# Optimization experiments

Hardware: AMD Instinct MI355X
Metric: run time of the kernel (lower is better)

Reference implementation:

```python
import jax, jax.numpy as jnp
import numpy as np

IN_DIM = 784
HIDDEN = 512
STYLE = 128
BATCH = 2048
NUM_LABELS = 10


def setup_inputs() -> dict:
    key = jax.random.key(0)
    k1, k2, k3, k4 = jax.random.split(key, 4)
    x = jax.random.uniform(k1, (BATCH, IN_DIM), dtype=jnp.float32)
    m = jax.random.randint(k2, (BATCH,), 0, NUM_LABELS)
    # Embedding tables, scaled as in the torch __init__ (N(0,1)/fan)
    fc1_table = jax.random.normal(k3, (NUM_LABELS, (IN_DIM + 1) * HIDDEN), dtype=jnp.float32) / ((IN_DIM + 1) * HIDDEN)
    fc2_table = jax.random.normal(k4, (NUM_LABELS, (HIDDEN + 1) * STYLE), dtype=jnp.float32) / ((HIDDEN + 1) * STYLE)
    return {"x": x, "m": m, "fc1_table": fc1_table, "fc2_table": fc2_table}


def reference(x, m, fc1_table, fc2_table):
    B = x.shape[0]
    x = x.reshape(B, -1)  # [B, 784]
    # Per-sample weight matrices gathered by label
    fc1 = fc1_table[m].reshape(B, IN_DIM + 1, HIDDEN)   # [B, 785, H]
    fc1_w, fc1_b = fc1[:, :IN_DIM, :], fc1[:, -1, :]
    h1 = jax.nn.relu(jnp.einsum('bkj,bk->bj', fc1_w, x) + fc1_b)  # [B, H]
    fc2 = fc2_table[m].reshape(B, HIDDEN + 1, STYLE)    # [B, H+1, S]
    fc2_w, fc2_b = fc2[:, :HIDDEN, :], fc2[:, -1, :]
    h2 = jnp.einsum('bkj,bk->bj', fc2_w, h1) + fc2_b    # [B, S]
    return jax.nn.sigmoid(h2)
```

## Files before the change

kernel.cpp:

```cpp
#include <hip/hip_runtime.h>
#include <hip/hip_bf16.h>
#include <math.h>

#define BATCH      2048
#define IN_DIM     784
#define HIDDEN     512
#define STYLE      128
#define NUM_LABELS 10
#define FC1_STRIDE ((IN_DIM + 1) * HIDDEN)
#define FC2_STRIDE ((HIDDEN + 1) * STYLE)
#define KP1        832
#define TB         64
#define BK         64
#define MAX_TILES  48

#define META_NTILES 31
#define META_TILES  32
#define META_PERM   176

#define W1B_OFF  16384ULL
#define W2B_OFF  (W1B_OFF + 10ULL*HIDDEN*KP1*2)
#define H1B_OFF  (W2B_OFF + 10ULL*STYLE*HIDDEN*2)
#define BF16_NEED (H1B_OFF + (size_t)BATCH*HIDDEN*2)

#define W1_KB 26
#define W1_NB 16
#define W2_KB 16
#define W2_NB 4
#define W1_BLOCKS (W1_KB*W1_NB*NUM_LABELS)
#define W2_BLOCKS (W2_KB*W2_NB*NUM_LABELS)

typedef short short8  __attribute__((ext_vector_type(8)));
typedef float float4e __attribute__((ext_vector_type(4)));

__device__ __forceinline__ ushort f2b(float v) {
    __hip_bfloat16 h = __float2bfloat16(v);
    return *reinterpret_cast<ushort*>(&h);
}

__global__ void k_prep(const int* __restrict__ m, const float* __restrict__ fc1t,
                       const float* __restrict__ fc2t, int* __restrict__ meta,
                       ushort* __restrict__ w1b, ushort* __restrict__ w2b) {
    const int tid = threadIdx.x;
    int bid = blockIdx.x;

    __shared__ int cnt[NUM_LABELS], curs[NUM_LABELS], offs[NUM_LABELS + 1];
    __shared__ int permS[BATCH];
    __shared__ float tile[32][33];

    if (bid == 0) {
        if (tid < NUM_LABELS) { cnt[tid] = 0; curs[tid] = 0; }
        __syncthreads();
        for (int b = tid; b < BATCH; b += 256) atomicAdd(&cnt[m[b]], 1);
        __syncthreads();
        if (tid == 0) {
            int off = 0;
            for (int L = 0; L < NUM_LABELS; ++L) { offs[L] = off; off += cnt[L]; }
            offs[NUM_LABELS] = off;
        }
        __syncthreads();
        for (int b = tid; b < BATCH; b += 256) {
            int L = m[b];
            int r = atomicAdd(&curs[L], 1);
            permS[offs[L] + r] = b;
        }
        __syncthreads();
        for (int i = tid; i < BATCH; i += 256) meta[META_PERM + i] = permS[i];
        if (tid == 0) {
            int idx = 0;
            for (int L = 0; L < NUM_LABELS; ++L) {
                int c = cnt[L], off = offs[L];
                for (int t = 0; t < c; t += TB) {
                    meta[META_TILES + idx * 3 + 0] = L;
                    meta[META_TILES + idx * 3 + 1] = off + t;
                    meta[META_TILES + idx * 3 + 2] = min(TB, c - t);
                    ++idx;
                }
            }
            meta[META_NTILES] = idx;
        }
        return;
    }

    bid -= 1;
    const float* src; ushort* dst; int Kvalid, Kpad, N, kb, nb, L; size_t srcL, dstL;
    if (bid < W1_BLOCKS) {
        kb = bid % W1_KB; nb = (bid / W1_KB) % W1_NB; L = bid / (W1_KB * W1_NB);
        src = fc1t; dst = w1b; Kvalid = IN_DIM; Kpad = KP1; N = HIDDEN;
        srcL = FC1_STRIDE; dstL = (size_t)HIDDEN * KP1;
    } else {
        bid -= W1_BLOCKS;
        kb = bid % W2_KB; nb = (bid / W2_KB) % W2_NB; L = bid / (W2_KB * W2_NB);
        src = fc2t; dst = w2b; Kvalid = HIDDEN; Kpad = HIDDEN; N = STYLE;
        srcL = FC2_STRIDE; dstL = (size_t)STYLE * HIDDEN;
    }
    const int tx = tid & 31, ty = tid >> 5;
    const int k0 = kb * 32, n0 = nb * 32;
    for (int r = ty; r < 32; r += 8) {
        int k = k0 + r;
        tile[r][tx] = (k < Kvalid) ? src[(size_t)L * srcL + (size_t)k * N + n0 + tx] : 0.f;
    }
    __syncthreads();
    for (int r = ty; r < 32; r += 8) {
        int n = n0 + r;
        dst[(size_t)L * dstL + (size_t)n * Kpad + k0 + tx] = f2b(tile[tx][r]);
    }
}

__launch_bounds__(256)
__global__ void k_fc1m(const float* __restrict__ x, const ushort* __restrict__ w1b,
                       const float* __restrict__ fc1t, const int* __restrict__ meta,
                       ushort* __restrict__ h1b) {
    const int t = blockIdx.x;
    if (t >= meta[META_NTILES]) return;
    const int L      = meta[META_TILES + 3 * t + 0];
    const int pstart = meta[META_TILES + 3 * t + 1];
    const int nrows  = meta[META_TILES + 3 * t + 2];
    const int col0   = blockIdx.y * 64;
    const ushort* __restrict__ W = w1b + (size_t)L * HIDDEN * KP1 + (size_t)col0 * KP1;

    __shared__ int rows[TB];
    __shared__ __align__(16) ushort As[64][72];
    __shared__ __align__(16) ushort Bs[64][72];

    const int tid = threadIdx.x;
    if (tid < TB) rows[tid] = (tid < nrows) ? meta[META_PERM + pstart + tid] : -1;
    __syncthreads();

    const int sr = tid >> 2, sc = tid & 3;
    const int lane = tid & 63, wv = tid >> 6;
    const int qd = lane >> 4, ln16 = lane & 15;

    const int arow = rows[sr];
    const float* __restrict__ xr = x + (size_t)(arow < 0 ? 0 : arow) * IN_DIM;
    const uint4* __restrict__ bgp = (const uint4*)(W + (size_t)sr * KP1);

    float4e acc[4] = {};

    float4 a0 = make_float4(0.f,0.f,0.f,0.f), a1 = a0, a2 = a0, a3 = a0;
    uint4 b0, b1;
    {
        const int ka = sc * 16;
        if (arow >= 0) {
            if (ka      < IN_DIM) a0 = *(const float4*)(xr + ka);
            if (ka + 4  < IN_DIM) a1 = *(const float4*)(xr + ka + 4);
            if (ka + 8  < IN_DIM) a2 = *(const float4*)(xr + ka + 8);
            if (ka + 12 < IN_DIM) a3 = *(const float4*)(xr + ka + 12);
        }
        b0 = bgp[sc * 2 + 0];
        b1 = bgp[sc * 2 + 1];
    }

    for (int k0 = 0; k0 < KP1; k0 += BK) {
        ushort av[16];
        av[0]=f2b(a0.x); av[1]=f2b(a0.y); av[2]=f2b(a0.z); av[3]=f2b(a0.w);
        av[4]=f2b(a1.x); av[5]=f2b(a1.y); av[6]=f2b(a1.z); av[7]=f2b(a1.w);
        av[8]=f2b(a2.x); av[9]=f2b(a2.y); av[10]=f2b(a2.z); av[11]=f2b(a2.w);
        av[12]=f2b(a3.x); av[13]=f2b(a3.y); av[14]=f2b(a3.z); av[15]=f2b(a3.w);
        *(uint4*)&As[sr][sc * 16 + 0] = *(const uint4*)&av[0];
        *(uint4*)&As[sr][sc * 16 + 8] = *(const uint4*)&av[8];
        *(uint4*)&Bs[sr][sc * 16 + 0] = b0;
        *(uint4*)&Bs[sr][sc * 16 + 8] = b1;
        __syncthreads();

        if (k0 + BK < KP1) {
            const int ka = k0 + BK + sc * 16;
            a0 = make_float4(0.f,0.f,0.f,0.f); a1 = a0; a2 = a0; a3 = a0;
            if (arow >= 0) {
                if (ka      < IN_DIM) a0 = *(const float4*)(xr + ka);
                if (ka + 4  < IN_DIM) a1 = *(const float4*)(xr + ka + 4);
                if (ka + 8  < IN_DIM) a2 = *(const float4*)(xr + ka + 8);
                if (ka + 12 < IN_DIM) a3 = *(const float4*)(xr + ka + 12);
            }
            b0 = bgp[((k0 + BK) >> 3) + sc * 2 + 0];
            b1 = bgp[((k0 + BK) >> 3) + sc * 2 + 1];
        }

#pragma unroll
        for (int s = 0; s < 2; ++s) {
            short8 af = *(const short8*)&As[wv * 16 + ln16][s * 32 + qd * 8];
#pragma unroll
            for (int nt = 0; nt < 4; ++nt) {
                short8 bf = *(const short8*)&Bs[nt * 16 + ln16][s * 32 + qd * 8];
                acc[nt] = __builtin_amdgcn_mfma_f32_16x16x32_bf16(af, bf, acc[nt], 0, 0, 0);
            }
        }
        __syncthreads();
    }

    const float* __restrict__ bias = fc1t + (size_t)L * FC1_STRIDE + (size_t)IN_DIM * HIDDEN + col0;
#pragma unroll
    for (int nt = 0; nt < 4; ++nt) {
        const int c = nt * 16 + ln16;
        const float bs = bias[c];
#pragma unroll
        for (int i = 0; i < 4; ++i) {
            const int r = wv * 16 + qd * 4 + i;
            if (r < nrows)
                h1b[(size_t)(pstart + r) * HIDDEN + col0 + c] = f2b(fmaxf(acc[nt][i] + bs, 0.f));
        }
    }
}

__launch_bounds__(256)
__global__ void k_fc2m(const ushort* __restrict__ h1b, const ushort* __restrict__ w2b,
                       const float* __restrict__ fc2t, const int* __restrict__ meta,
                       float* __restrict__ out) {
    const int t = blockIdx.x;
    if (t >= meta[META_NTILES]) return;
    const int L      = meta[META_TILES + 3 * t + 0];
    const int pstart = meta[META_TILES + 3 * t + 1];
    const int nrows  = meta[META_TILES + 3 * t + 2];
    const int col0   = blockIdx.y * 64;
    const ushort* __restrict__ W = w2b + (size_t)L * STYLE * HIDDEN + (size_t)col0 * HIDDEN;

    __shared__ int rows[TB];
    __shared__ __align__(16) ushort As[64][72];
    __shared__ __align__(16) ushort Bs[64][72];

    const int tid = threadIdx.x;
    if (tid < TB) rows[tid] = (tid < nrows) ? meta[META_PERM + pstart + tid] : -1;
    __syncthreads();

    const int sr = tid >> 2, sc = tid & 3;
    const int lane = tid & 63, wv = tid >> 6;
    const int qd = lane >> 4, ln16 = lane & 15;

    const bool aval = (sr < nrows);
    const uint4* __restrict__ agp = (const uint4*)(h1b + (size_t)(pstart + (aval ? sr : 0)) * HIDDEN);
    const uint4* __restrict__ bgp = (const uint4*)(W + (size_t)sr * HIDDEN);

    float4e acc[4] = {};

    uint4 a0 = make_uint4(0u,0u,0u,0u), a1 = a0, b0, b1;
    if (aval) { a0 = agp[sc * 2 + 0]; a1 = agp[sc * 2 + 1]; }
    b0 = bgp[sc * 2 + 0];
    b1 = bgp[sc * 2 + 1];

    for (int k0 = 0; k0 < HIDDEN; k0 += BK) {
        *(uint4*)&As[sr][sc * 16 + 0] = a0;
        *(uint4*)&As[sr][sc * 16 + 8] = a1;
        *(uint4*)&Bs[sr][sc * 16 + 0] = b0;
        *(uint4*)&Bs[sr][sc * 16 + 8] = b1;
        __syncthreads();

        if (k0 + BK < HIDDEN) {
            const int base = ((k0 + BK) >> 3) + sc * 2;
            a0 = make_uint4(0u,0u,0u,0u); a1 = a0;
            if (aval) { a0 = agp[base]; a1 = agp[base + 1]; }
            b0 = bgp[base];
            b1 = bgp[base + 1];
        }

#pragma unroll
        for (int s = 0; s < 2; ++s) {
            short8 af = *(const short8*)&As[wv * 16 + ln16][s * 32 + qd * 8];
#pragma unroll
            for (int nt = 0; nt < 4; ++nt) {
                short8 bf = *(const short8*)&Bs[nt * 16 + ln16][s * 32 + qd * 8];
                acc[nt] = __builtin_amdgcn_mfma_f32_16x16x32_bf16(af, bf, acc[nt], 0, 0, 0);
            }
        }
        __syncthreads();
    }

    const float* __restrict__ bias = fc2t + (size_t)L * FC2_STRIDE + (size_t)HIDDEN * STYLE + col0;
#pragma unroll
    for (int nt = 0; nt < 4; ++nt) {
        const int c = nt * 16 + ln16;
        const float bs = bias[c];
#pragma unroll
        for (int i = 0; i < 4; ++i) {
            const int r = wv * 16 + qd * 4 + i;
            if (r < nrows) {
                const int orow = rows[r];
                out[(size_t)orow * STYLE + col0 + c] = 1.f / (1.f + __expf(-(acc[nt][i] + bs)));
            }
        }
    }
}

__launch_bounds__(256)
__global__ void k_naive(const float* __restrict__ x, const int* __restrict__ m,
                        const float* __restrict__ fc1t, const float* __restrict__ fc2t,
                        float* __restrict__ out) {
    __shared__ float xs[IN_DIM];
    __shared__ float h1[HIDDEN];
    const int b = blockIdx.x, tid = threadIdx.x, L = m[b];
    for (int k = tid; k < IN_DIM; k += 256) xs[k] = x[(size_t)b * IN_DIM + k];
    __syncthreads();
    const float* __restrict__ W1 = fc1t + (size_t)L * FC1_STRIDE;
    for (int j = tid; j < HIDDEN; j += 256) {
        float acc = W1[(size_t)IN_DIM * HIDDEN + j];
        for (int k = 0; k < IN_DIM; ++k) acc = fmaf(xs[k], W1[(size_t)k * HIDDEN + j], acc);
        h1[j] = fmaxf(acc, 0.f);
    }
    __syncthreads();
    const float* __restrict__ W2 = fc2t + (size_t)L * FC2_STRIDE;
    for (int j = tid; j < STYLE; j += 256) {
        float acc = W2[(size_t)HIDDEN * STYLE + j];
        for (int k = 0; k < HIDDEN; ++k) acc = fmaf(h1[k], W2[(size_t)k * STYLE + j], acc);
        out[(size_t)b * STYLE + j] = 1.f / (1.f + __expf(-acc));
    }
}

extern "C" void kernel_launch(void* const* d_in, const int* in_sizes, int n_in,
                              void* d_out, int out_size, void* d_ws, size_t ws_size,
                              hipStream_t stream) {
    const float* x    = (const float*)d_in[0];
    const int*   m    = (const int*)d_in[1];
    const float* fc1t = (const float*)d_in[2];
    const float* fc2t = (const float*)d_in[3];
    float* out = (float*)d_out;

    if (ws_size >= BF16_NEED) {
        int*    meta = (int*)d_ws;
        ushort* w1b  = (ushort*)((char*)d_ws + W1B_OFF);
        ushort* w2b  = (ushort*)((char*)d_ws + W2B_OFF);
        ushort* h1b  = (ushort*)((char*)d_ws + H1B_OFF);

        k_prep<<<1 + W1_BLOCKS + W2_BLOCKS, 256, 0, stream>>>(m, fc1t, fc2t, meta, w1b, w2b);
        k_fc1m<<<dim3(MAX_TILES, HIDDEN / 64), 256, 0, stream>>>(x, w1b, fc1t, meta, h1b);
        k_fc2m<<<dim3(MAX_TILES, STYLE / 64), 256, 0, stream>>>(h1b, w2b, fc2t, meta, out);
    } else {
        k_naive<<<BATCH, 256, 0, stream>>>(x, m, fc1t, fc2t, out);
    }
}
```

Baseline: 103.3 us.

## Drop prep kernel: compute label tiles per block and convert weights in-loop

Removes the separate prep kernel that sorted rows by label and pre-transposed both weight tables to bf16. Each GEMM block now recomputes the label histogram, tile assignment and its row list from m using ballots and a shared-memory scan. It reads fp32 weights directly, transposing and converting them while staging into LDS. The k-loop also becomes double-buffered with a single barrier per step. This saves one launch and the full weight conversion pass, at the cost of redundant per-block metadata work and twice the global bytes for weight loads.

After: 116.2 us. +12.5%, slower.

```diff
diff --git a/kernel.cpp b/kernel.cpp
--- a/kernel.cpp
+++ b/kernel.cpp
@@ -14,21 +14,7 @@
 #define BK         64
 #define MAX_TILES  48
 
-#define META_NTILES 31
-#define META_TILES  32
-#define META_PERM   176
-
-#define W1B_OFF  16384ULL
-#define W2B_OFF  (W1B_OFF + 10ULL*HIDDEN*KP1*2)
-#define H1B_OFF  (W2B_OFF + 10ULL*STYLE*HIDDEN*2)
-#define BF16_NEED (H1B_OFF + (size_t)BATCH*HIDDEN*2)
-
-#define W1_KB 26
-#define W1_NB 16
-#define W2_KB 16
-#define W2_NB 4
-#define W1_BLOCKS (W1_KB*W1_NB*NUM_LABELS)
-#define W2_BLOCKS (W2_KB*W2_NB*NUM_LABELS)
+#define WS_NEED  ((size_t)BATCH * HIDDEN * 2)
 
 typedef short short8  __attribute__((ext_vector_type(8)));
 typedef float float4e __attribute__((ext_vector_type(4)));
@@ -38,157 +24,154 @@
     return *reinterpret_cast<ushort*>(&h);
 }
 
-__global__ void k_prep(const int* __restrict__ m, const float* __restrict__ fc1t,
-                       const float* __restrict__ fc2t, int* __restrict__ meta,
-                       ushort* __restrict__ w1b, ushort* __restrict__ w2b) {
+__device__ __forceinline__ bool block_meta(const int* __restrict__ m, int bt,
+                                           int* cntS, int* scanS, int* rowsS,
+                                           int& L, int& pstart, int& nrows) {
     const int tid = threadIdx.x;
-    int bid = blockIdx.x;
-
-    __shared__ int cnt[NUM_LABELS], curs[NUM_LABELS], offs[NUM_LABELS + 1];
-    __shared__ int permS[BATCH];
-    __shared__ float tile[32][33];
-
-    if (bid == 0) {
-        if (tid < NUM_LABELS) { cnt[tid] = 0; curs[tid] = 0; }
+    int mloc[8];
+#pragma unroll
+    for (int i = 0; i < 8; ++i) mloc[i] = m[tid * 8 + i];
+
+    if (tid < NUM_LABELS) cntS[tid] = 0;
+    __syncthreads();
+#pragma unroll
+    for (int i = 0; i < 8; ++i) {
+        const int v = mloc[i];
+#pragma unroll
+        for (int Li = 0; Li < NUM_LABELS; ++Li) {
+            unsigned long long bal = __ballot(v == Li);
+            if ((tid & 63) == 0) atomicAdd(&cntS[Li], (int)__popcll(bal));
+        }
+    }
+    __syncthreads();
+
+    L = -1; pstart = 0; nrows = 0; int t = 0;
+    {
+        int off = 0, idx = 0;
+        for (int Li = 0; Li < NUM_LABELS; ++Li) {
+            const int c = cntS[Li];
+            const int nt = (c + TB - 1) >> 6;
+            if (L < 0 && bt >= idx && bt < idx + nt) {
+                L = Li; t = bt - idx;
+                pstart = off + t * TB;
+                nrows = min(TB, c - t * TB);
+            }
+            idx += nt; off += c;
+        }
+    }
+    if (L < 0) return false;
+
+    int loc = 0;
+#pragma unroll
+    for (int i = 0; i < 8; ++i) loc += (mloc[i] == L);
+    scanS[tid] = loc;
+    __syncthreads();
+    for (int s = 1; s < 256; s <<= 1) {
+        int v = scanS[tid];
+        int u = (tid >= s) ? scanS[tid - s] : 0;
         __syncthreads();
-        for (int b = tid; b < BATCH; b += 256) atomicAdd(&cnt[m[b]], 1);
+        scanS[tid] = v + u;
         __syncthreads();
-        if (tid == 0) {
-            int off = 0;
-            for (int L = 0; L < NUM_LABELS; ++L) { offs[L] = off; off += cnt[L]; }
-            offs[NUM_LABELS] = off;
-        }
-        __syncthreads();
-        for (int b = tid; b < BATCH; b += 256) {
-            int L = m[b];
-            int r = atomicAdd(&curs[L], 1);
-            permS[offs[L] + r] = b;
-        }
-        __syncthreads();
-        for (int i = tid; i < BATCH; i += 256) meta[META_PERM + i] = permS[i];
-        if (tid == 0) {
-            int idx = 0;
-            for (int L = 0; L < NUM_LABELS; ++L) {
-                int c = cnt[L], off = offs[L];
-                for (int t = 0; t < c; t += TB) {
-                    meta[META_TILES + idx * 3 + 0] = L;
-                    meta[META_TILES + idx * 3 + 1] = off + t;
-                    meta[META_TILES + idx * 3 + 2] = min(TB, c - t);
-                    ++idx;
-                }
-            }
-            meta[META_NTILES] = idx;
-        }
-        return;
-    }
-
-    bid -= 1;
-    const float* src; ushort* dst; int Kvalid, Kpad, N, kb, nb, L; size_t srcL, dstL;
-    if (bid < W1_BLOCKS) {
-        kb = bid % W1_KB; nb = (bid / W1_KB) % W1_NB; L = bid / (W1_KB * W1_NB);
-        src = fc1t; dst = w1b; Kvalid = IN_DIM; Kpad = KP1; N = HIDDEN;
-        srcL = FC1_STRIDE; dstL = (size_t)HIDDEN * KP1;
-    } else {
-        bid -= W1_BLOCKS;
-        kb = bid % W2_KB; nb = (bid / W2_KB) % W2_NB; L = bid / (W2_KB * W2_NB);
-        src = fc2t; dst = w2b; Kvalid = HIDDEN; Kpad = HIDDEN; N = STYLE;
-        srcL = FC2_STRIDE; dstL = (size_t)STYLE * HIDDEN;
-    }
-    const int tx = tid & 31, ty = tid >> 5;
-    const int k0 = kb * 32, n0 = nb * 32;
-    for (int r = ty; r < 32; r += 8) {
-        int k = k0 + r;
-        tile[r][tx] = (k < Kvalid) ? src[(size_t)L * srcL + (size_t)k * N + n0 + tx] : 0.f;
-    }
-    __syncthreads();
-    for (int r = ty; r < 32; r += 8) {
-        int n = n0 + r;
-        dst[(size_t)L * dstL + (size_t)n * Kpad + k0 + tx] = f2b(tile[tx][r]);
-    }
+    }
+    const int base = (tid > 0) ? scanS[tid - 1] : 0;
+    if (tid < TB) rowsS[tid] = -1;
+    __syncthreads();
+    const int lo = t * TB, hi = lo + TB;
+    int r = base;
+#pragma unroll
+    for (int i = 0; i < 8; ++i) {
+        if (mloc[i] == L) {
+            if (r >= lo && r < hi) rowsS[r - lo] = tid * 8 + i;
+            ++r;
+        }
+    }
+    __syncthreads();
+    return true;
 }
 
 __launch_bounds__(256)
-__global__ void k_fc1m(const float* __restrict__ x, const ushort* __restrict__ w1b,
-                       const float* __restrict__ fc1t, const int* __restrict__ meta,
-                       ushort* __restrict__ h1b) {
-    const int t = blockIdx.x;
-    if (t >= meta[META_NTILES]) return;
-    const int L      = meta[META_TILES + 3 * t + 0];
-    const int pstart = meta[META_TILES + 3 * t + 1];
-    const int nrows  = meta[META_TILES + 3 * t + 2];
-    const int col0   = blockIdx.y * 64;
-    const ushort* __restrict__ W = w1b + (size_t)L * HIDDEN * KP1 + (size_t)col0 * KP1;
-
-    __shared__ int rows[TB];
-    __shared__ __align__(16) ushort As[64][72];
-    __shared__ __align__(16) ushort Bs[64][72];
+__global__ void k_fc1m(const float* __restrict__ x, const int* __restrict__ m,
+                       const float* __restrict__ fc1t, ushort* __restrict__ h1b) {
+    __shared__ int cntS[NUM_LABELS], scanS[256], rowsS[TB];
+    __shared__ __align__(16) ushort As[2][64][72];
+    __shared__ __align__(16) ushort Bs[2][64][72];
+
+    int L, pstart, nrows;
+    if (!block_meta(m, blockIdx.x, cntS, scanS, rowsS, L, pstart, nrows)) return;
+    const int col0 = blockIdx.y * 64;
+    const float* __restrict__ W = fc1t + (size_t)L * FC1_STRIDE;
 
     const int tid = threadIdx.x;
-    if (tid < TB) rows[tid] = (tid < nrows) ? meta[META_PERM + pstart + tid] : -1;
-    __syncthreads();
-
     const int sr = tid >> 2, sc = tid & 3;
+    const int kq = tid >> 4, nq = tid & 15;
     const int lane = tid & 63, wv = tid >> 6;
     const int qd = lane >> 4, ln16 = lane & 15;
 
-    const int arow = rows[sr];
+    const int arow = rowsS[sr];
     const float* __restrict__ xr = x + (size_t)(arow < 0 ? 0 : arow) * IN_DIM;
-    const uint4* __restrict__ bgp = (const uint4*)(W + (size_t)sr * KP1);
 
     float4e acc[4] = {};
-
-    float4 a0 = make_float4(0.f,0.f,0.f,0.f), a1 = a0, a2 = a0, a3 = a0;
-    uint4 b0, b1;
-    {
-        const int ka = sc * 16;
+    float4 a0, a1, a2, a3;
+    float4 bw[4];
+
+    auto loadA = [&](int k0) {
+        const int ka = k0 + sc * 16;
+        a0 = make_float4(0.f,0.f,0.f,0.f); a1 = a0; a2 = a0; a3 = a0;
         if (arow >= 0) {
             if (ka      < IN_DIM) a0 = *(const float4*)(xr + ka);
             if (ka + 4  < IN_DIM) a1 = *(const float4*)(xr + ka + 4);
             if (ka + 8  < IN_DIM) a2 = *(const float4*)(xr + ka + 8);
             if (ka + 12 < IN_DIM) a3 = *(const float4*)(xr + ka + 12);
         }
-        b0 = bgp[sc * 2 + 0];
-        b1 = bgp[sc * 2 + 1];
-    }
-
-    for (int k0 = 0; k0 < KP1; k0 += BK) {
+    };
+    auto loadB = [&](int k0) {
+#pragma unroll
+        for (int kk = 0; kk < 4; ++kk) {
+            const int gk = k0 + kq * 4 + kk;
+            bw[kk] = (gk < IN_DIM) ? *(const float4*)(W + (size_t)gk * HIDDEN + col0 + nq * 4)
+                                   : make_float4(0.f,0.f,0.f,0.f);
+        }
+    };
+    auto storeA = [&](int p) {
         ushort av[16];
         av[0]=f2b(a0.x); av[1]=f2b(a0.y); av[2]=f2b(a0.z); av[3]=f2b(a0.w);
         av[4]=f2b(a1.x); av[5]=f2b(a1.y); av[6]=f2b(a1.z); av[7]=f2b(a1.w);
         av[8]=f2b(a2.x); av[9]=f2b(a2.y); av[10]=f2b(a2.z); av[11]=f2b(a2.w);
         av[12]=f2b(a3.x); av[13]=f2b(a3.y); av[14]=f2b(a3.z); av[15]=f2b(a3.w);
-        *(uint4*)&As[sr][sc * 16 + 0] = *(const uint4*)&av[0];
-        *(uint4*)&As[sr][sc * 16 + 8] = *(const uint4*)&av[8];
-        *(uint4*)&Bs[sr][sc * 16 + 0] = b0;
-        *(uint4*)&Bs[sr][sc * 16 + 8] = b1;
+        *(uint4*)&As[p][sr][sc * 16 + 0] = *(const uint4*)&av[0];
+        *(uint4*)&As[p][sr][sc * 16 + 8] = *(const uint4*)&av[8];
+    };
+    auto storeB = [&](int p) {
+#pragma unroll
+        for (int nn = 0; nn < 4; ++nn) {
+            ushort kv[4] = { f2b((&bw[0].x)[nn]), f2b((&bw[1].x)[nn]),
+                             f2b((&bw[2].x)[nn]), f2b((&bw[3].x)[nn]) };
+            *(uint2*)&Bs[p][nq * 4 + nn][kq * 4] = *(const uint2*)kv;
+        }
+    };
+
+    loadA(0); loadB(0);
+    storeA(0); storeB(0);
+    loadA(BK); loadB(BK);
+
+    int p = 0;
+    for (int k0 = 0; k0 < KP1; k0 += BK) {
         __syncthreads();
-
-        if (k0 + BK < KP1) {
-            const int ka = k0 + BK + sc * 16;
-            a0 = make_float4(0.f,0.f,0.f,0.f); a1 = a0; a2 = a0; a3 = a0;
-            if (arow >= 0) {
-                if (ka      < IN_DIM) a0 = *(const float4*)(xr + ka);
-                if (ka + 4  < IN_DIM) a1 = *(const float4*)(xr + ka + 4);
-                if (ka + 8  < IN_DIM) a2 = *(const float4*)(xr + ka + 8);
-                if (ka + 12 < IN_DIM) a3 = *(const float4*)(xr + ka + 12);
-            }
-            b0 = bgp[((k0 + BK) >> 3) + sc * 2 + 0];
-            b1 = bgp[((k0 + BK) >> 3) + sc * 2 + 1];
-        }
-
+        if (k0 + BK < KP1) { storeA(1 - p); storeB(1 - p); }
+        if (k0 + 2 * BK < KP1) { loadA(k0 + 2 * BK); loadB(k0 + 2 * BK); }
 #pragma unroll
         for (int s = 0; s < 2; ++s) {
-            short8 af = *(const short8*)&As[wv * 16 + ln16][s * 32 + qd * 8];
+            short8 af = *(const short8*)&As[p][wv * 16 + ln16][s * 32 + qd * 8];
 #pragma unroll
             for (int nt = 0; nt < 4; ++nt) {
-                short8 bf = *(const short8*)&Bs[nt * 16 + ln16][s * 32 + qd * 8];
+                short8 bf = *(const short8*)&Bs[p][nt * 16 + ln16][s * 32 + qd * 8];
                 acc[nt] = __builtin_amdgcn_mfma_f32_16x16x32_bf16(af, bf, acc[nt], 0, 0, 0);
             }
         }
-        __syncthreads();
-    }
-
-    const float* __restrict__ bias = fc1t + (size_t)L * FC1_STRIDE + (size_t)IN_DIM * HIDDEN + col0;
+        p ^= 1;
+    }
+
+    const float* __restrict__ bias = W + (size_t)IN_DIM * HIDDEN + col0;
 #pragma unroll
     for (int nt = 0; nt < 4; ++nt) {
         const int c = nt * 16 + ln16;
@@ -203,68 +186,77 @@
 }
 
 __launch_bounds__(256)
-__global__ void k_fc2m(const ushort* __restrict__ h1b, const ushort* __restrict__ w2b,
-                       const float* __restrict__ fc2t, const int* __restrict__ meta,
-                       float* __restrict__ out) {
-    const int t = blockIdx.x;
-    if (t >= meta[META_NTILES]) return;
-    const int L      = meta[META_TILES + 3 * t + 0];
-    const int pstart = meta[META_TILES + 3 * t + 1];
-    const int nrows  = meta[META_TILES + 3 * t + 2];
-    const int col0   = blockIdx.y * 64;
-    const ushort* __restrict__ W = w2b + (size_t)L * STYLE * HIDDEN + (size_t)col0 * HIDDEN;
-
-    __shared__ int rows[TB];
-    __shared__ __align__(16) ushort As[64][72];
-    __shared__ __align__(16) ushort Bs[64][72];
+__global__ void k_fc2m(const ushort* __restrict__ h1b, const int* __restrict__ m,
+                       const float* __restrict__ fc2t, float* __restrict__ out) {
+    __shared__ int cntS[NUM_LABELS], scanS[256], rowsS[TB];
+    __shared__ __align__(16) ushort As[2][64][72];
+    __shared__ __align__(16) ushort Bs[2][64][72];
+
+    int L, pstart, nrows;
+    if (!block_meta(m, blockIdx.x, cntS, scanS, rowsS, L, pstart, nrows)) return;
+    const int col0 = blockIdx.y * 64;
+    const float* __restrict__ W = fc2t + (size_t)L * FC2_STRIDE;
 
     const int tid = threadIdx.x;
-    if (tid < TB) rows[tid] = (tid < nrows) ? meta[META_PERM + pstart + tid] : -1;
-    __syncthreads();
-
     const int sr = tid >> 2, sc = tid & 3;
+    const int kq = tid >> 4, nq = tid & 15;
     const int lane = tid & 63, wv = tid >> 6;
     const int qd = lane >> 4, ln16 = lane & 15;
 
     const bool aval = (sr < nrows);
     const uint4* __restrict__ agp = (const uint4*)(h1b + (size_t)(pstart + (aval ? sr : 0)) * HIDDEN);
-    const uint4* __restrict__ bgp = (const uint4*)(W + (size_t)sr * HIDDEN);
 
     float4e acc[4] = {};
-
-    uint4 a0 = make_uint4(0u,0u,0u,0u), a1 = a0, b0, b1;
-    if (aval) { a0 = agp[sc * 2 + 0]; a1 = agp[sc * 2 + 1]; }
-    b0 = bgp[sc * 2 + 0];
-    b1 = bgp[sc * 2 + 1];
-
+    uint4 a0, a1;
+    float4 bw[4];
+
+    auto loadA = [&](int k0) {
+        const int base = (k0 >> 3) + sc * 2;
+        a0 = make_uint4(0u,0u,0u,0u); a1 = a0;
+        if (aval) { a0 = agp[base]; a1 = agp[base + 1]; }
+    };
+    auto loadB = [&](int k0) {
+#pragma unroll
+        for (int kk = 0; kk < 4; ++kk) {
+            const int gk = k0 + kq * 4 + kk;
+            bw[kk] = *(const float4*)(W + (size_t)gk * STYLE + col0 + nq * 4);
+        }
+    };
+    auto storeA = [&](int p) {
+        *(uint4*)&As[p][sr][sc * 16 + 0] = a0;
+        *(uint4*)&As[p][sr][sc * 16 + 8] = a1;
+    };
+    auto storeB = [&](int p) {
+#pragma unroll
+        for (int nn = 0; nn < 4; ++nn) {
+            ushort kv[4] = { f2b((&bw[0].x)[nn]), f2b((&bw[1].x)[nn]),
+                             f2b((&bw[2].x)[nn]), f2b((&bw[3].x)[nn]) };
+            *(uint2*)&Bs[p][nq * 4 + nn][kq * 4] = *(const uint2*)kv;
+        }
+    };
+
+    loadA(0); loadB(0);
+    storeA(0); storeB(0);
+    loadA(BK); loadB(BK);
+
+    int p = 0;
     for (int k0 = 0; k0 < HIDDEN; k0 += BK) {
-        *(uint4*)&As[sr][sc * 16 + 0] = a0;
-        *(uint4*)&As[sr][sc * 16 + 8] = a1;
-        *(uint4*)&Bs[sr][sc * 16 + 0] = b0;
-        *(uint4*)&Bs[sr][sc * 16 + 8] = b1;
         __syncthreads();
-
-        if (k0 + BK < HIDDEN) {
-            const int base = ((k0 + BK) >> 3) + sc * 2;
-            a0 = make_uint4(0u,0u,0u,0u); a1 = a0;
-            if (aval) { a0 = agp[base]; a1 = agp[base + 1]; }
-            b0 = bgp[base];
-            b1 = bgp[base + 1];
-        }
-
+        if (k0 + BK < HIDDEN) { storeA(1 - p); storeB(1 - p); }
+        if (k0 + 2 * BK < HIDDEN) { loadA(k0 + 2 * BK); loadB(k0 + 2 * BK); }
 #pragma unroll
         for (int s = 0; s < 2; ++s) {
-            short8 af = *(const short8*)&As[wv * 16 + ln16][s * 32 + qd * 8];
+            short8 af = *(const short8*)&As[p][wv * 16 + ln16][s * 32 + qd * 8];
 #pragma unroll
             for (int nt = 0; nt < 4; ++nt) {
-                short8 bf = *(const short8*)&Bs[nt * 16 + ln16][s * 32 + qd * 8];
+                short8 bf = *(const short8*)&Bs[p][nt * 16 + ln16][s * 32 + qd * 8];
                 acc[nt] = __builtin_amdgcn_mfma_f32_16x16x32_bf16(af, bf, acc[nt], 0, 0, 0);
             }
         }
-        __syncthreads();
-    }
-
-    const float* __restrict__ bias = fc2t + (size_t)L * FC2_STRIDE + (size_t)HIDDEN * STYLE + col0;
+        p ^= 1;
+    }
+
+    const float* __restrict__ bias = W + (size_t)HIDDEN * STYLE + col0;
 #pragma unroll
     for (int nt = 0; nt < 4; ++nt) {
         const int c = nt * 16 + ln16;
@@ -273,7 +265,7 @@
         for (int i = 0; i < 4; ++i) {
             const int r = wv * 16 + qd * 4 + i;
             if (r < nrows) {
-                const int orow = rows[r];
+                const int orow = rowsS[r];
                 out[(size_t)orow * STYLE + col0 + c] = 1.f / (1.f + __expf(-(acc[nt][i] + bs)));
             }
         }
@@ -313,15 +305,10 @@
     const float* fc2t = (const float*)d_in[3];
     float* out = (float*)d_out;
 
-    if (ws_size >= BF16_NEED) {
-        int*    meta = (int*)d_ws;
-        ushort* w1b  = (ushort*)((char*)d_ws + W1B_OFF);
-        ushort* w2b  = (ushort*)((char*)d_ws + W2B_OFF);
-        ushort* h1b  = (ushort*)((char*)d_ws + H1B_OFF);
-
-        k_prep<<<1 + W1_BLOCKS + W2_BLOCKS, 256, 0, stream>>>(m, fc1t, fc2t, meta, w1b, w2b);
-        k_fc1m<<<dim3(MAX_TILES, HIDDEN / 64), 256, 0, stream>>>(x, w1b, fc1t, meta, h1b);
-        k_fc2m<<<dim3(MAX_TILES, STYLE / 64), 256, 0, stream>>>(h1b, w2b, fc2t, meta, out);
+    if (ws_size >= WS_NEED) {
+        ushort* h1b = (ushort*)d_ws;
+        k_fc1m<<<dim3(MAX_TILES, HIDDEN / 64), 256, 0, stream>>>(x, m, fc1t, h1b);
+        k_fc2m<<<dim3(MAX_TILES, STYLE / 64), 256, 0, stream>>>(h1b, m, fc2t, out);
     } else {
         k_naive<<<BATCH, 256, 0, stream>>>(x, m, fc1t, fc2t, out);
     }
```
